# Kernel optimization log

Hardware: AMD Instinct MI355X
Metric: run time of the kernel (lower is better)

Reference implementation:

```python
import jax, jax.numpy as jnp
import numpy as np

B, L, D, H = 4, 1024, 1024, 16
DH = D // H
NEG = -1e9
EPS = 1e-5


def setup_inputs() -> dict:
    key = jax.random.key(0)
    ks = jax.random.split(key, 12)
    s = 1.0 / np.sqrt(D)
    inp = {
        "Q": jax.random.normal(ks[0], (B, L, D), jnp.float32),
        "K": jax.random.normal(ks[1], (B, L, D), jnp.float32),
        "V": jax.random.normal(ks[2], (B, L, D), jnp.float32),
        "K_mask": jnp.ones((B, L), jnp.int32),
        "WQ": jax.random.normal(ks[3], (D, D), jnp.float32) * s,
        "bQ": jnp.zeros((D,), jnp.float32),
        "WK": jax.random.normal(ks[4], (D, D), jnp.float32) * s,
        "bK": jnp.zeros((D,), jnp.float32),
        "WV": jax.random.normal(ks[5], (D, D), jnp.float32) * s,
        "bV": jnp.zeros((D,), jnp.float32),
        "WO": jax.random.normal(ks[6], (D, D), jnp.float32) * s,
        "bO": jnp.zeros((D,), jnp.float32),
        "ln_g": jnp.ones((D,), jnp.float32),
        "ln_b": jnp.zeros((D,), jnp.float32),
    }
    return inp


def _mha(Q, K, V, K_mask, WQ, bQ, WK, bK, WV, bV, WO, bO, ln_g, ln_b):
    # projections  [B,L,D]
    q = Q @ WQ + bQ
    k = K @ WK + bK
    v = V @ WV + bV
    # split heads -> [B,H,L,dh]
    q = q.reshape(B, L, H, DH).transpose(0, 2, 1, 3)
    k = k.reshape(B, L, H, DH).transpose(0, 2, 1, 3)
    v = v.reshape(B, L, H, DH).transpose(0, 2, 1, 3)
    # scaled dot product, masked softmax over keys
    scores = jnp.einsum("bhqd,bhkd->bhqk", q, k) / jnp.sqrt(jnp.float32(DH))
    mask = (K_mask > 0)[:, None, None, :]  # [B,1,1,Lk]
    scores = jnp.where(mask, scores, NEG)
    attn = jax.nn.softmax(scores, axis=-1)  # dropout is identity at inference
    ctx = jnp.einsum("bhqk,bhkd->bhqd", attn, v)
    ctx = ctx.transpose(0, 2, 1, 3).reshape(B, L, D)
    # output layer: dense + residual + layernorm
    out = ctx @ WO + bO
    x = out + Q
    mu = jnp.mean(x, axis=-1, keepdims=True)
    var = jnp.var(x, axis=-1, keepdims=True)
    return (x - mu) * jax.lax.rsqrt(var + EPS) * ln_g + ln_b


def reference(Q, K, V, K_mask, WQ, bQ, WK, bK, WV, bV, WO, bO, ln_g, ln_b):
    return _mha(Q, K, V, K_mask, WQ, bQ, WK, bK, WV, bV, WO, bO, ln_g, ln_b)
```

## Files before the change

kernel.cpp:

```cpp
#include <hip/hip_runtime.h>
#include <hip/hip_bf16.h>
#include <stdint.h>

#define Bn 4
#define Ln 1024
#define Dn 1024
#define Hn 16
#define DHn 64
#define Mn (Bn*Ln)

typedef __attribute__((ext_vector_type(8))) short short8v;
typedef __attribute__((ext_vector_type(4))) float floatx4;

__device__ __forceinline__ unsigned short f2b(float f){
  union { float f; unsigned u; } v; v.f = f;
  unsigned r = (v.u + 0x7FFFu + ((v.u >> 16) & 1u)) >> 16;
  return (unsigned short)r;
}
__device__ __forceinline__ unsigned short f2b_fast(float f){
  __hip_bfloat16 h = __float2bfloat16(f);
  return *reinterpret_cast<unsigned short*>(&h);
}

typedef const unsigned __attribute__((address_space(1)))* gas1_t;
typedef unsigned __attribute__((address_space(3)))* las3_t;
__device__ __forceinline__ void gload16(const void* g, void* l){
  __builtin_amdgcn_global_load_lds((gas1_t)(uintptr_t)g, (las3_t)(uintptr_t)l, 16, 0, 0);
}

__global__ __launch_bounds__(256) void tobf16x3_k(const float* __restrict__ x0,
    const float* __restrict__ x1, const float* __restrict__ x2,
    unsigned short* __restrict__ o0, unsigned short* __restrict__ o1,
    unsigned short* __restrict__ o2)
{
  const int i = blockIdx.x * 256 + threadIdx.x;
  const int sel = i >> 20, idx = i & 0xFFFFF;
  const float* x = sel == 0 ? x0 : (sel == 1 ? x1 : x2);
  unsigned short* o = sel == 0 ? o0 : (sel == 1 ? o1 : o2);
  float4 v = reinterpret_cast<const float4*>(x)[idx];
  union { unsigned short u[4]; uint2 q; } p;
  p.u[0] = f2b(v.x); p.u[1] = f2b(v.y); p.u[2] = f2b(v.z); p.u[3] = f2b(v.w);
  reinterpret_cast<uint2*>(o)[idx] = p.q;
}

__global__ __launch_bounds__(256) void wconv4_k(const float* __restrict__ W0,
    const float* __restrict__ W1, const float* __restrict__ W2,
    const float* __restrict__ W3, unsigned short* __restrict__ Wt0,
    unsigned short* __restrict__ Wt1, unsigned short* __restrict__ Wt2,
    unsigned short* __restrict__ Wt3)
{
  const float* W; unsigned short* Wt;
  switch (blockIdx.z){
    case 0: W = W0; Wt = Wt0; break;
    case 1: W = W1; Wt = Wt1; break;
    case 2: W = W2; Wt = Wt2; break;
    default: W = W3; Wt = Wt3; break;
  }
  __shared__ float tile[64][65];
  const int nb = blockIdx.x * 64, kb = blockIdx.y * 64;
  const int tx = threadIdx.x & 63, ty = threadIdx.x >> 6;
  #pragma unroll
  for (int r = 0; r < 64; r += 4)
    tile[r + ty][tx] = W[(size_t)(kb + r + ty) * 1024 + nb + tx];
  __syncthreads();
  #pragma unroll
  for (int r = 0; r < 64; r += 4)
    Wt[(size_t)(nb + r + ty) * 1024 + kb + tx] = f2b(tile[tx][r + ty]);
}

template<int MODE>
__device__ __forceinline__ void gemm8_core(const unsigned short* __restrict__ Ab,
    const unsigned short* __restrict__ Btp, const float* __restrict__ bias,
    void* __restrict__ outp, float scale, unsigned short* lds, int nt, int mt)
{
  const int tid = threadIdx.x;
  const int lane = tid & 63, wave = tid >> 6;
  const int wr = wave >> 2, wc = wave & 3;
  const int lg = lane >> 4, lr = lane & 15;
  const int m0 = mt * 256, n0 = nt * 256;

  const unsigned short* gAb[2];
  const unsigned short* gBb[2];
  int ldso[2];
  #pragma unroll
  for (int i = 0; i < 2; i++){
    int c = tid + 512 * i;
    int g16 = c >> 6, lrr = c & 15, lgg = (c >> 4) & 3;
    int row = g16 * 16 + lrr;
    gAb[i] = Ab  + (size_t)(m0 + row) * 1024 + lgg * 8;
    gBb[i] = Btp + (size_t)(n0 + row) * 1024 + lgg * 8;
    ldso[i] = c * 8;
  }
  auto stageA = [&](int sg){
    unsigned short* slot = lds + (sg & 3) * 16384;
    const int kcol = (sg >> 1) * 64 + (sg & 1) * 32;
    #pragma unroll
    for (int i = 0; i < 2; i++) gload16(gAb[i] + kcol, &slot[ldso[i]]);
  };
  auto stageB = [&](int sg){
    unsigned short* slot = lds + (sg & 3) * 16384 + 8192;
    const int kcol = (sg >> 1) * 64 + (sg & 1) * 32;
    #pragma unroll
    for (int i = 0; i < 2; i++) gload16(gBb[i] + kcol, &slot[ldso[i]]);
  };

  floatx4 acc[8][4] = {};

  stageA(0); stageB(0); stageA(1); stageB(1); stageA(2); stageB(2);

  for (int t = 0; t < 16; t++){
    unsigned short* slot0 = lds + ((2 * t) & 3) * 16384;
    unsigned short* slot1 = lds + ((2 * t + 1) & 3) * 16384;
    short8v af[4], bf[4];
    if (t < 15) asm volatile("s_waitcnt vmcnt(4)" ::: "memory");
    else        asm volatile("s_waitcnt vmcnt(0)" ::: "memory");
    __builtin_amdgcn_s_barrier();
    __builtin_amdgcn_sched_barrier(0);
    if (t < 15) stageA(2 * t + 3);
    #pragma unroll
    for (int n = 0; n < 4; n++)
      bf[n] = *reinterpret_cast<const short8v*>(&slot0[8192 + ((wc * 4 + n) * 64 + lane) * 8]);
    #pragma unroll
    for (int i2 = 0; i2 < 4; i2++)
      af[i2] = *reinterpret_cast<const short8v*>(&slot0[((wr * 8 + i2) * 64 + lane) * 8]);
    __builtin_amdgcn_s_setprio(1);
    #pragma unroll
    for (int a = 0; a < 4; a++)
      #pragma unroll
      for (int n = 0; n < 4; n++)
        acc[a][n] = __builtin_amdgcn_mfma_f32_16x16x32_bf16(af[a], bf[n], acc[a][n], 0, 0, 0);
    __builtin_amdgcn_s_setprio(0);
    if (t < 15) stageB(2 * t + 3);
    #pragma unroll
    for (int i2 = 0; i2 < 4; i2++)
      af[i2] = *reinterpret_cast<const short8v*>(&slot0[((wr * 8 + 4 + i2) * 64 + lane) * 8]);
    __builtin_amdgcn_s_setprio(1);
    #pragma unroll
    for (int a = 0; a < 4; a++)
      #pragma unroll
      for (int n = 0; n < 4; n++)
        acc[4 + a][n] = __builtin_amdgcn_mfma_f32_16x16x32_bf16(af[a], bf[n], acc[4 + a][n], 0, 0, 0);
    __builtin_amdgcn_s_setprio(0);
    __builtin_amdgcn_sched_barrier(0);
    __builtin_amdgcn_s_barrier();
    __builtin_amdgcn_sched_barrier(0);
    if (t < 14) stageA(2 * t + 4);
    #pragma unroll
    for (int n = 0; n < 4; n++)
      bf[n] = *reinterpret_cast<const short8v*>(&slot1[8192 + ((wc * 4 + n) * 64 + lane) * 8]);
    #pragma unroll
    for (int i2 = 0; i2 < 4; i2++)
      af[i2] = *reinterpret_cast<const short8v*>(&slot1[((wr * 8 + i2) * 64 + lane) * 8]);
    __builtin_amdgcn_s_setprio(1);
    #pragma unroll
    for (int a = 0; a < 4; a++)
      #pragma unroll
      for (int n = 0; n < 4; n++)
        acc[a][n] = __builtin_amdgcn_mfma_f32_16x16x32_bf16(af[a], bf[n], acc[a][n], 0, 0, 0);
    __builtin_amdgcn_s_setprio(0);
    if (t < 14) stageB(2 * t + 4);
    #pragma unroll
    for (int i2 = 0; i2 < 4; i2++)
      af[i2] = *reinterpret_cast<const short8v*>(&slot1[((wr * 8 + 4 + i2) * 64 + lane) * 8]);
    __builtin_amdgcn_s_setprio(1);
    #pragma unroll
    for (int a = 0; a < 4; a++)
      #pragma unroll
      for (int n = 0; n < 4; n++)
        acc[4 + a][n] = __builtin_amdgcn_mfma_f32_16x16x32_bf16(af[a], bf[n], acc[4 + a][n], 0, 0, 0);
    __builtin_amdgcn_s_setprio(0);
    __builtin_amdgcn_sched_barrier(0);
  }

  if constexpr (MODE == 2){
    __syncthreads();
    #pragma unroll
    for (int n = 0; n < 4; n++){
      const int gn_l = wc * 64 + n * 16 + lr;
      const float bb = bias[n0 + gn_l];
      const int X = (gn_l & 7) << 3;
      #pragma unroll
      for (int a = 0; a < 8; a++){
        const int gm_l = wr * 128 + a * 16 + lg * 4;
        union { unsigned short u[4]; uint2 q; } pk;
        #pragma unroll
        for (int r = 0; r < 4; r++) pk.u[r] = f2b((acc[a][n][r] + bb) * scale);
        *reinterpret_cast<uint2*>(&lds[gn_l * 256 + (gm_l ^ X)]) = pk.q;
      }
    }
    __syncthreads();
    const int bb2 = m0 >> 10, l0 = m0 & 1023;
    const int row = tid >> 1, colb = (tid & 1) * 128;
    const int h2 = (n0 + row) >> 6, d = (n0 + row) & 63;
    unsigned short* obase = (unsigned short*)outp +
        (((size_t)(bb2 * Hn + h2)) * DHn + d) * Ln + l0 + colb;
    const int XR = (row & 7) << 3;
    #pragma unroll
    for (int g = 0; g < 16; g++){
      short8v v = *reinterpret_cast<const short8v*>(&lds[row * 256 + ((colb + g * 8) ^ XR)]);
      *reinterpret_cast<short8v*>(obase + g * 8) = v;
    }
  } else {
    unsigned short* o = (unsigned short*)outp;
    #pragma unroll
    for (int n = 0; n < 4; n++){
      const int gn = n0 + wc * 64 + n * 16 + lr;
      const float bbv = bias[gn];
      const int h2 = gn >> 6, d = gn & 63;
      #pragma unroll
      for (int a = 0; a < 8; a++){
        const int gm0v = m0 + wr * 128 + a * 16 + lg * 4;
        #pragma unroll
        for (int r = 0; r < 4; r++){
          const int gm = gm0v + r;
          const int bb2 = gm >> 10, l = gm & 1023;
          o[(((size_t)(bb2 * Hn + h2)) * Ln + l) * DHn + d] = f2b((acc[a][n][r] + bbv) * scale);
        }
      }
    }
  }
}

__global__ __launch_bounds__(512, 2) void gemmqkv8_k(
    const unsigned short* __restrict__ A0, const unsigned short* __restrict__ A1,
    const unsigned short* __restrict__ A2, const unsigned short* __restrict__ W0,
    const unsigned short* __restrict__ W1, const unsigned short* __restrict__ W2,
    const float* __restrict__ b0, const float* __restrict__ b1,
    const float* __restrict__ b2, unsigned short* __restrict__ o0,
    unsigned short* __restrict__ o1, unsigned short* __restrict__ o2, float qscl)
{
  __shared__ __align__(16) unsigned short lds[65536];
  const int g = blockIdx.x >> 3;
  const int nt = g & 3;
  const int panel = (g >> 2) * 8 + (blockIdx.x & 7);
  const int z = panel >> 4, mt = panel & 15;
  if (z == 0)
    gemm8_core<0>(A0, W0, b0, o0, qscl, lds, nt, mt);
  else if (z == 1)
    gemm8_core<0>(A1, W1, b1, o1, 1.f, lds, nt, mt);
  else
    gemm8_core<2>(A2, W2, b2, o2, 1.f, lds, nt, mt);
}

__global__ __launch_bounds__(256) void gemmo_k(const unsigned short* __restrict__ Ab,
    const unsigned short* __restrict__ W, const float* __restrict__ bias,
    float* __restrict__ out, const float* __restrict__ resid)
{
  __shared__ __align__(16) unsigned short lds[32768];
  const int bid = blockIdx.x;
  const int xcd = bid & 7, k = bid >> 3;
  const int mt = xcd * 4 + (k >> 3);
  const int nt = k & 7;

  const int tid = threadIdx.x;
  const int lane = tid & 63, wave = tid >> 6;
  const int wr = wave >> 1, wc = wave & 1;
  const int lg = lane >> 4, lr = lane & 15;
  const int m0 = mt * 128, n0 = nt * 128;

  const unsigned short* gA[2];
  const unsigned short* gB[2];
  int ldso[2];
  #pragma unroll
  for (int i = 0; i < 2; i++){
    int c = tid + 256 * i;
    int g16 = c >> 6, lrr = c & 15, lgg = (c >> 4) & 3;
    int row = g16 * 16 + lrr;
    gA[i] = Ab + (size_t)(m0 + row) * 1024 + lgg * 8;
    gB[i] = W  + (size_t)(n0 + row) * 1024 + lgg * 8;
    ldso[i] = c * 8;
  }
  auto issue = [&](int s){
    unsigned short* base = lds + (s & 3) * 8192;
    const int kc = s * 32;
    #pragma unroll
    for (int i = 0; i < 2; i++) gload16(gA[i] + kc, &base[ldso[i]]);
    #pragma unroll
    for (int i = 0; i < 2; i++) gload16(gB[i] + kc, &base[4096 + ldso[i]]);
  };

  floatx4 acc[4][4] = {};

  issue(0); issue(1); issue(2);

  for (int s = 0; s < 32; s++){
    unsigned short* base = lds + (s & 3) * 8192;
    if (s <= 29)      asm volatile("s_waitcnt vmcnt(8)" ::: "memory");
    else if (s == 30) asm volatile("s_waitcnt vmcnt(4)" ::: "memory");
    else              asm volatile("s_waitcnt vmcnt(0)" ::: "memory");
    __builtin_amdgcn_s_barrier();
    __builtin_amdgcn_sched_barrier(0);
    if (s <= 28) issue(s + 3);
    short8v af[4], bf[4];
    #pragma unroll
    for (int m = 0; m < 4; m++)
      af[m] = *reinterpret_cast<const short8v*>(&base[((wr * 4 + m) * 64 + lane) * 8]);
    #pragma unroll
    for (int n = 0; n < 4; n++)
      bf[n] = *reinterpret_cast<const short8v*>(&base[4096 + ((wc * 4 + n) * 64 + lane) * 8]);
    __builtin_amdgcn_s_setprio(1);
    #pragma unroll
    for (int m = 0; m < 4; m++)
      #pragma unroll
      for (int n = 0; n < 4; n++)
        acc[m][n] = __builtin_amdgcn_mfma_f32_16x16x32_bf16(af[m], bf[n], acc[m][n], 0, 0, 0);
    __builtin_amdgcn_s_setprio(0);
    __builtin_amdgcn_sched_barrier(0);
  }

  #pragma unroll
  for (int n = 0; n < 4; n++){
    const int gn = n0 + wc * 64 + n * 16 + lr;
    const float bb = bias[gn];
    #pragma unroll
    for (int m = 0; m < 4; m++){
      const int gm0 = m0 + wr * 64 + m * 16 + lg * 4;
      #pragma unroll
      for (int r = 0; r < 4; r++){
        const int gm = gm0 + r;
        out[(size_t)gm * Dn + gn] = acc[m][n][r] + bb + resid[(size_t)gm * Dn + gn];
      }
    }
  }
}

__global__ __launch_bounds__(256) void attn_k(const unsigned short* __restrict__ qb,
    const unsigned short* __restrict__ kbf, const unsigned short* __restrict__ vtb,
    const int* __restrict__ kmask, unsigned short* __restrict__ ctx)
{
  const int bh = blockIdx.x;
  const int qt = blockIdx.y;
  const int b = bh >> 4, h = bh & 15;
  const int tid = threadIdx.x;
  const int w = tid >> 6, lane = tid & 63;
  const int lg = lane >> 4, lr = lane & 15;

  const unsigned short* qp = qb  + (size_t)bh * Ln * DHn;
  const unsigned short* kp = kbf + (size_t)bh * Ln * DHn;
  const unsigned short* vp = vtb + (size_t)bh * DHn * Ln;
  const int q0 = qt * 128 + w * 32;

  __shared__ __align__(16) unsigned short ldsK[2][4096];
  __shared__ __align__(16) unsigned short ldsV[2][4096];
  __shared__ __align__(16) unsigned short plds[4][32][72];

  const unsigned short* gK[2];
  const unsigned short* gV[2];
  #pragma unroll
  for (int i = 0; i < 2; i++){
    int bc = w * 2 + i;
    int ks = bc >> 2, j = bc & 3;
    int row = j * 16 + lr, col = ks * 32 + lg * 8;
    gK[i] = kp + (size_t)row * DHn + col;
    gV[i] = vp + (size_t)row * Ln  + col;
  }

  short8v aq[2][2];
  #pragma unroll
  for (int f = 0; f < 2; f++)
    #pragma unroll
    for (int ks = 0; ks < 2; ks++)
      aq[f][ks] = *reinterpret_cast<const short8v*>(
          qp + (size_t)(q0 + f * 16 + lr) * DHn + ks * 32 + lg * 8);

  floatx4 accO[2][4] = {};
  float lsacc[2][4] = {{0.f,0.f,0.f,0.f},{0.f,0.f,0.f,0.f}};

  const int* mrow = kmask + b * Ln;
  int mkA[4], mkB[4];

  #pragma unroll
  for (int i = 0; i < 2; i++){
    gload16(gK[i], &ldsK[0][(w * 2 + i) * 512]);
    gload16(gV[i], &ldsV[0][(w * 2 + i) * 512]);
  }
  #pragma unroll
  for (int j = 0; j < 4; j++) mkA[j] = mrow[j * 16 + lr];

  for (int t = 0; t < 16; t++){
    const int cur = t & 1;
    asm volatile("s_waitcnt vmcnt(0)" ::: "memory");
    __syncthreads();
    if (t < 15){
      #pragma unroll
      for (int i = 0; i < 2; i++){
        gload16(gK[i] + (size_t)(t + 1) * 4096, &ldsK[cur ^ 1][(w * 2 + i) * 512]);
        gload16(gV[i] + (size_t)(t + 1) * 64,   &ldsV[cur ^ 1][(w * 2 + i) * 512]);
      }
      #pragma unroll
      for (int j = 0; j < 4; j++) mkB[j] = mrow[(t + 1) * 64 + j * 16 + lr];
    }

    floatx4 s[2][4] = {};
    #pragma unroll
    for (int ks = 0; ks < 2; ks++)
      #pragma unroll
      for (int j = 0; j < 4; j++){
        short8v bk = *reinterpret_cast<const short8v*>(&ldsK[cur][((ks * 4 + j) * 64 + lane) * 8]);
        s[0][j] = __builtin_amdgcn_mfma_f32_16x16x32_bf16(aq[0][ks], bk, s[0][j], 0, 0, 0);
        s[1][j] = __builtin_amdgcn_mfma_f32_16x16x32_bf16(aq[1][ks], bk, s[1][j], 0, 0, 0);
      }
    if (__all(mkA[0] > 0 && mkA[1] > 0 && mkA[2] > 0 && mkA[3] > 0)){
      #pragma unroll
      for (int f = 0; f < 2; f++)
        #pragma unroll
        for (int j = 0; j < 4; j++)
          #pragma unroll
          for (int r = 0; r < 4; r++){
            float p = __builtin_amdgcn_exp2f(s[f][j][r]);
            lsacc[f][r] += p;
            plds[w][f * 16 + lg * 4 + r][j * 16 + lr] = f2b_fast(p);
          }
    } else {
      #pragma unroll
      for (int j = 0; j < 4; j++){
        const float madd = mkA[j] > 0 ? 0.f : -1e9f;
        #pragma unroll
        for (int f = 0; f < 2; f++)
          #pragma unroll
          for (int r = 0; r < 4; r++){
            float p = __builtin_amdgcn_exp2f(s[f][j][r] + madd);
            lsacc[f][r] += p;
            plds[w][f * 16 + lg * 4 + r][j * 16 + lr] = f2b_fast(p);
          }
      }
    }
    #pragma unroll
    for (int ks = 0; ks < 2; ks++){
      short8v pa0 = *reinterpret_cast<const short8v*>(&plds[w][lr][ks * 32 + lg * 8]);
      short8v pa1 = *reinterpret_cast<const short8v*>(&plds[w][16 + lr][ks * 32 + lg * 8]);
      #pragma unroll
      for (int n = 0; n < 4; n++){
        short8v bv = *reinterpret_cast<const short8v*>(&ldsV[cur][((ks * 4 + n) * 64 + lane) * 8]);
        accO[0][n] = __builtin_amdgcn_mfma_f32_16x16x32_bf16(pa0, bv, accO[0][n], 0, 0, 0);
        accO[1][n] = __builtin_amdgcn_mfma_f32_16x16x32_bf16(pa1, bv, accO[1][n], 0, 0, 0);
      }
    }
    #pragma unroll
    for (int j = 0; j < 4; j++) mkA[j] = mkB[j];
  }

  #pragma unroll
  for (int f = 0; f < 2; f++)
    #pragma unroll
    for (int r = 0; r < 4; r++){
      lsacc[f][r] += __shfl_xor(lsacc[f][r], 1, 64);
      lsacc[f][r] += __shfl_xor(lsacc[f][r], 2, 64);
      lsacc[f][r] += __shfl_xor(lsacc[f][r], 4, 64);
      lsacc[f][r] += __shfl_xor(lsacc[f][r], 8, 64);
      lsacc[f][r] = 1.f / fmaxf(lsacc[f][r], 1e-20f);
    }
  #pragma unroll
  for (int f = 0; f < 2; f++)
    #pragma unroll
    for (int n = 0; n < 4; n++)
      #pragma unroll
      for (int r = 0; r < 4; r++){
        float o = accO[f][n][r] * lsacc[f][r];
        int q = q0 + f * 16 + lg * 4 + r;
        ctx[((size_t)(b * Ln + q)) * Dn + h * DHn + n * 16 + lr] = f2b_fast(o);
      }
}

__global__ __launch_bounds__(256) void ln_k(const float* __restrict__ x,
    const float* __restrict__ g, const float* __restrict__ bt, float* __restrict__ out)
{
  const int row = blockIdx.x;
  const int tid = threadIdx.x;
  float4 v = *reinterpret_cast<const float4*>(x + (size_t)row * 1024 + tid * 4);
  float s  = v.x + v.y + v.z + v.w;
  float sq = v.x * v.x + v.y * v.y + v.z * v.z + v.w * v.w;
  #pragma unroll
  for (int off = 32; off >= 1; off >>= 1){
    s  += __shfl_xor(s, off, 64);
    sq += __shfl_xor(sq, off, 64);
  }
  __shared__ float psm[4], pqm[4];
  const int w = tid >> 6;
  if ((tid & 63) == 0){ psm[w] = s; pqm[w] = sq; }
  __syncthreads();
  s  = psm[0] + psm[1] + psm[2] + psm[3];
  sq = pqm[0] + pqm[1] + pqm[2] + pqm[3];
  const float mean = s * (1.f / 1024.f);
  const float var  = sq * (1.f / 1024.f) - mean * mean;
  const float inv  = rsqrtf(var + 1e-5f);
  float4 gg = *reinterpret_cast<const float4*>(g  + tid * 4);
  float4 bb = *reinterpret_cast<const float4*>(bt + tid * 4);
  float4 o;
  o.x = (v.x - mean) * inv * gg.x + bb.x;
  o.y = (v.y - mean) * inv * gg.y + bb.y;
  o.z = (v.z - mean) * inv * gg.z + bb.z;
  o.w = (v.w - mean) * inv * gg.w + bb.w;
  *reinterpret_cast<float4*>(out + (size_t)row * 1024 + tid * 4) = o;
}

extern "C" void kernel_launch(void* const* d_in, const int* in_sizes, int n_in,
                              void* d_out, int out_size, void* d_ws, size_t ws_size,
                              hipStream_t stream)
{
  const float* Qin = (const float*)d_in[0];
  const float* Kin = (const float*)d_in[1];
  const float* Vin = (const float*)d_in[2];
  const int*   Kms = (const int*)d_in[3];
  const float* WQ  = (const float*)d_in[4];
  const float* bQ  = (const float*)d_in[5];
  const float* WK  = (const float*)d_in[6];
  const float* bK  = (const float*)d_in[7];
  const float* WV  = (const float*)d_in[8];
  const float* bV  = (const float*)d_in[9];
  const float* WO  = (const float*)d_in[10];
  const float* bO  = (const float*)d_in[11];
  const float* lng = (const float*)d_in[12];
  const float* lnb = (const float*)d_in[13];

  char* ws = (char*)d_ws;
  const size_t MB = 1024u * 1024u;
  unsigned short* wqt = (unsigned short*)(ws + 0 * MB);
  unsigned short* wkt = (unsigned short*)(ws + 2 * MB);
  unsigned short* wvt = (unsigned short*)(ws + 4 * MB);
  unsigned short* wot = (unsigned short*)(ws + 6 * MB);
  unsigned short* qbf = (unsigned short*)(ws + 8 * MB);
  unsigned short* kbf = (unsigned short*)(ws + 16 * MB);
  unsigned short* vtb = (unsigned short*)(ws + 24 * MB);
  unsigned short* ctx = (unsigned short*)(ws + 32 * MB);
  float*          xbf = (float*)(ws + 40 * MB);
  unsigned short* cv0 = (unsigned short*)(ws + 32 * MB);
  unsigned short* cv1 = (unsigned short*)(ws + 40 * MB);
  unsigned short* cv2 = (unsigned short*)(ws + 48 * MB);

  dim3 blk(256);
  wconv4_k<<<dim3(16, 16, 4), blk, 0, stream>>>(WQ, WK, WV, WO, wqt, wkt, wvt, wot);
  tobf16x3_k<<<12288, blk, 0, stream>>>(Qin, Kin, Vin, cv0, cv1, cv2);

  const float QSCL = 0.125f * 1.44269504088896f;
  gemmqkv8_k<<<192, dim3(512), 0, stream>>>(cv0, cv1, cv2, wqt, wkt, wvt,
                                            bQ, bK, bV, qbf, kbf, vtb, QSCL);

  attn_k<<<dim3(64, 8), blk, 0, stream>>>(qbf, kbf, vtb, Kms, ctx);

  gemmo_k<<<256, blk, 0, stream>>>(ctx, wot, bO, xbf, Qin);

  ln_k<<<4096, blk, 0, stream>>>(xbf, lng, lnb, (float*)d_out);
}
```

Before: 120.4 us.

## Merge prep kernels and stage Q/K and ctx stores through LDS for 16-byte writes

Combines the weight transpose-convert and the activation bf16-convert kernels into one launch, removing a kernel boundary. In the QKV GEMM epilogue for the row-major head layout and in the attention output, results are first written into a per-wave LDS patch and then stored to global memory as 16-byte vectors instead of scattered 2-byte stores. The aim is better write coalescing and less launch overhead, at the cost of extra LDS traffic and reliance on the LDS regions (plds, the gemm lds buffer) being free at that point.

```diff
diff --git a/kernel.cpp b/kernel.cpp
--- a/kernel.cpp
+++ b/kernel.cpp
@@ -28,44 +28,44 @@
   __builtin_amdgcn_global_load_lds((gas1_t)(uintptr_t)g, (las3_t)(uintptr_t)l, 16, 0, 0);
 }
 
-__global__ __launch_bounds__(256) void tobf16x3_k(const float* __restrict__ x0,
+__global__ __launch_bounds__(256) void prep_k(const float* __restrict__ W0,
+    const float* __restrict__ W1, const float* __restrict__ W2,
+    const float* __restrict__ W3, unsigned short* __restrict__ Wt0,
+    unsigned short* __restrict__ Wt1, unsigned short* __restrict__ Wt2,
+    unsigned short* __restrict__ Wt3, const float* __restrict__ x0,
     const float* __restrict__ x1, const float* __restrict__ x2,
     unsigned short* __restrict__ o0, unsigned short* __restrict__ o1,
     unsigned short* __restrict__ o2)
 {
-  const int i = blockIdx.x * 256 + threadIdx.x;
-  const int sel = i >> 20, idx = i & 0xFFFFF;
-  const float* x = sel == 0 ? x0 : (sel == 1 ? x1 : x2);
-  unsigned short* o = sel == 0 ? o0 : (sel == 1 ? o1 : o2);
-  float4 v = reinterpret_cast<const float4*>(x)[idx];
-  union { unsigned short u[4]; uint2 q; } p;
-  p.u[0] = f2b(v.x); p.u[1] = f2b(v.y); p.u[2] = f2b(v.z); p.u[3] = f2b(v.w);
-  reinterpret_cast<uint2*>(o)[idx] = p.q;
-}
-
-__global__ __launch_bounds__(256) void wconv4_k(const float* __restrict__ W0,
-    const float* __restrict__ W1, const float* __restrict__ W2,
-    const float* __restrict__ W3, unsigned short* __restrict__ Wt0,
-    unsigned short* __restrict__ Wt1, unsigned short* __restrict__ Wt2,
-    unsigned short* __restrict__ Wt3)
-{
-  const float* W; unsigned short* Wt;
-  switch (blockIdx.z){
-    case 0: W = W0; Wt = Wt0; break;
-    case 1: W = W1; Wt = Wt1; break;
-    case 2: W = W2; Wt = Wt2; break;
-    default: W = W3; Wt = Wt3; break;
-  }
   __shared__ float tile[64][65];
-  const int nb = blockIdx.x * 64, kb = blockIdx.y * 64;
-  const int tx = threadIdx.x & 63, ty = threadIdx.x >> 6;
-  #pragma unroll
-  for (int r = 0; r < 64; r += 4)
-    tile[r + ty][tx] = W[(size_t)(kb + r + ty) * 1024 + nb + tx];
-  __syncthreads();
-  #pragma unroll
-  for (int r = 0; r < 64; r += 4)
-    Wt[(size_t)(nb + r + ty) * 1024 + kb + tx] = f2b(tile[tx][r + ty]);
+  if (blockIdx.x < 1024){
+    const int z = blockIdx.x >> 8, rem = blockIdx.x & 255;
+    const float* W; unsigned short* Wt;
+    switch (z){
+      case 0: W = W0; Wt = Wt0; break;
+      case 1: W = W1; Wt = Wt1; break;
+      case 2: W = W2; Wt = Wt2; break;
+      default: W = W3; Wt = Wt3; break;
+    }
+    const int nb = (rem & 15) * 64, kb = (rem >> 4) * 64;
+    const int tx = threadIdx.x & 63, ty = threadIdx.x >> 6;
+    #pragma unroll
+    for (int r = 0; r < 64; r += 4)
+      tile[r + ty][tx] = W[(size_t)(kb + r + ty) * 1024 + nb + tx];
+    __syncthreads();
+    #pragma unroll
+    for (int r = 0; r < 64; r += 4)
+      Wt[(size_t)(nb + r + ty) * 1024 + kb + tx] = f2b(tile[tx][r + ty]);
+  } else {
+    const int i = (blockIdx.x - 1024) * 256 + threadIdx.x;
+    const int sel = i >> 20, idx = i & 0xFFFFF;
+    const float* x = sel == 0 ? x0 : (sel == 1 ? x1 : x2);
+    unsigned short* o = sel == 0 ? o0 : (sel == 1 ? o1 : o2);
+    float4 v = reinterpret_cast<const float4*>(x)[idx];
+    union { unsigned short u[4]; uint2 q; } p;
+    p.u[0] = f2b(v.x); p.u[1] = f2b(v.y); p.u[2] = f2b(v.z); p.u[3] = f2b(v.w);
+    reinterpret_cast<uint2*>(o)[idx] = p.q;
+  }
 }
 
 template<int MODE>
@@ -201,21 +201,28 @@
       *reinterpret_cast<short8v*>(obase + g * 8) = v;
     }
   } else {
+    unsigned short* plw = lds + wave * 1152;
     unsigned short* o = (unsigned short*)outp;
-    #pragma unroll
-    for (int n = 0; n < 4; n++){
-      const int gn = n0 + wc * 64 + n * 16 + lr;
-      const float bbv = bias[gn];
-      const int h2 = gn >> 6, d = gn & 63;
-      #pragma unroll
-      for (int a = 0; a < 8; a++){
-        const int gm0v = m0 + wr * 128 + a * 16 + lg * 4;
+    const int gnb = n0 + wc * 64;
+    const int h2 = gnb >> 6;
+    float bb4[4];
+    #pragma unroll
+    for (int n = 0; n < 4; n++) bb4[n] = bias[gnb + n * 16 + lr];
+    #pragma unroll
+    for (int a = 0; a < 8; a++){
+      #pragma unroll
+      for (int n = 0; n < 4; n++)
         #pragma unroll
-        for (int r = 0; r < 4; r++){
-          const int gm = gm0v + r;
-          const int bb2 = gm >> 10, l = gm & 1023;
-          o[(((size_t)(bb2 * Hn + h2)) * Ln + l) * DHn + d] = f2b((acc[a][n][r] + bbv) * scale);
-        }
+        for (int r = 0; r < 4; r++)
+          plw[(lg * 4 + r) * 72 + n * 16 + lr] = f2b((acc[a][n][r] + bb4[n]) * scale);
+      #pragma unroll
+      for (int it = 0; it < 2; it++){
+        const int row = it * 8 + (lane >> 3);
+        const int c   = lane & 7;
+        const int gm  = m0 + wr * 128 + a * 16 + row;
+        const int b2 = gm >> 10, l = gm & 1023;
+        short8v v = *reinterpret_cast<const short8v*>(&plw[row * 72 + c * 8]);
+        *reinterpret_cast<short8v*>(o + (((size_t)(b2 * Hn + h2)) * Ln + l) * DHn + c * 8) = v;
       }
     }
   }
@@ -455,11 +462,16 @@
     #pragma unroll
     for (int n = 0; n < 4; n++)
       #pragma unroll
-      for (int r = 0; r < 4; r++){
-        float o = accO[f][n][r] * lsacc[f][r];
-        int q = q0 + f * 16 + lg * 4 + r;
-        ctx[((size_t)(b * Ln + q)) * Dn + h * DHn + n * 16 + lr] = f2b_fast(o);
-      }
+      for (int r = 0; r < 4; r++)
+        plds[w][f * 16 + lg * 4 + r][n * 16 + lr] = f2b_fast(accO[f][n][r] * lsacc[f][r]);
+  #pragma unroll
+  for (int it = 0; it < 4; it++){
+    const int row = it * 8 + (lane >> 3);
+    const int c = lane & 7;
+    const int q = q0 + row;
+    short8v v = *reinterpret_cast<const short8v*>(&plds[w][row][c * 8]);
+    *reinterpret_cast<short8v*>(ctx + ((size_t)(b * Ln + q)) * Dn + h * DHn + c * 8) = v;
+  }
 }
 
 __global__ __launch_bounds__(256) void ln_k(const float* __restrict__ x,
@@ -529,8 +541,8 @@
   unsigned short* cv2 = (unsigned short*)(ws + 48 * MB);
 
   dim3 blk(256);
-  wconv4_k<<<dim3(16, 16, 4), blk, 0, stream>>>(WQ, WK, WV, WO, wqt, wkt, wvt, wot);
-  tobf16x3_k<<<12288, blk, 0, stream>>>(Qin, Kin, Vin, cv0, cv1, cv2);
+  prep_k<<<13312, blk, 0, stream>>>(WQ, WK, WV, WO, wqt, wkt, wvt, wot,
+                                    Qin, Kin, Vin, cv0, cv1, cv2);
 
   const float QSCL = 0.125f * 1.44269504088896f;
   gemmqkv8_k<<<192, dim3(512), 0, stream>>>(cv0, cv1, cv2, wqt, wkt, wvt,
```

Result: no change. 118.1 us (-1.9%).
